# Performance work log

Hardware: AMD Instinct MI355X
Metric: run time of the kernel (lower is better)

## Reference

```python
import jax, jax.numpy as jnp
import numpy as np

EPS = 1e-6


def setup_inputs() -> dict:
    key = jax.random.key(0)
    k1, k2, k3, k4, k5, k6 = jax.random.split(key, 6)
    B, S = 32, 1024
    H, W = 32, 32            # max_n_patches_h/w
    C, P = 3, 16             # channels, patch_res
    D = C * P * P            # 768
    P2 = P * P               # 256
    patches = jax.random.normal(k1, (B, S, D), dtype=jnp.float32)
    pos_h = jax.random.randint(k2, (B, S), 0, H)
    pos_w = jax.random.randint(k3, (B, S), 0, W)
    key_pad_mask = jax.random.bernoulli(k4, 0.1, (B, S))  # True where padding
    n = jnp.zeros((H, W), dtype=jnp.float32)
    mean = 0.1 * jax.random.normal(k5, (H, W, P2), dtype=jnp.float32)
    m2 = jax.random.uniform(k6, (H, W, P2), dtype=jnp.float32)
    return {"patches": patches, "pos_h": pos_h, "pos_w": pos_w,
            "key_pad_mask": key_pad_mask, "n": n, "mean": mean, "m2": m2}


def reference(patches, pos_h, pos_w, key_pad_mask, n, mean, m2):
    """PatchNorm.forward in training mode (Welford update + normalize).

    Masked (padded) positions contribute 0 to the scatter sums and are
    written back as zeros, matching the torch boolean-mask gather/scatter.
    """
    H, W, P2 = mean.shape
    B, S, D = patches.shape
    C = D // P2
    HW = H * W

    x = patches.reshape(B * S, C, P2)                    # (N, c, p^2)
    pf = (pos_h * W + pos_w).reshape(-1)                 # (N,) flat grid index
    w = (~key_pad_mask).reshape(-1).astype(patches.dtype)  # 1.0 on valid tokens

    # --- Welford online update (torch scatter_add semantics w/ duplicates) ---
    counts = jax.ops.segment_sum(w, pf, num_segments=HW)
    n_new = n + counts.reshape(H, W)

    mean_flat = mean.reshape(HW, P2)
    delta = (x - mean_flat[pf][:, None, :]).mean(axis=1) * w[:, None]  # (N, p^2)
    n_g = jnp.maximum(n_new.reshape(HW)[pf], 1.0)
    mean_new_flat = mean_flat + jax.ops.segment_sum(delta / n_g[:, None], pf, num_segments=HW)
    mean_new = mean_new_flat.reshape(H, W, P2)

    delta2 = (x - mean_new_flat[pf][:, None, :]).mean(axis=1) * w[:, None]
    m2_new = m2 + jax.ops.segment_sum(delta * delta2, pf, num_segments=HW).reshape(H, W, P2)

    # --- var / std (var := 1 where n < 2) ---
    var = jnp.where((n_new < 2.0)[..., None], 1.0,
                    m2_new / jnp.maximum(n_new, 1.0)[..., None])
    std = jnp.sqrt(var)

    # --- normalize with gathered per-position stats, zero out padding ---
    mg = mean_new.reshape(HW, P2)[pf][:, None, :]        # (N, 1, p^2)
    sg = std.reshape(HW, P2)[pf][:, None, :]
    out = (x - mg) / (sg + EPS) * w[:, None, None]
    return out.reshape(B, S, D)
```

## Files before the change

### kernel.cpp

```cpp
#include <hip/hip_runtime.h>
#include <math.h>


#define EPSF 1e-6f

static constexpr int W_GRID  = 32;
static constexpr int P2      = 256;
static constexpr int P4      = 64;
static constexpr int D4      = 192;
static constexpr int HW      = 1024;
static constexpr int NTOK    = 32768;
static constexpr int LISTCAP = 96;
static constexpr int SLICE   = NTOK / HW;

__global__ void k_pf(const int* __restrict__ pos_h,
                     const int* __restrict__ pos_w,
                     const int* __restrict__ mask,
                     unsigned short* __restrict__ pf16) {
    int i = blockIdx.x * blockDim.x + threadIdx.x;
    if (i >= NTOK) return;
    const int valid = (mask[i] == 0);
    pf16[i] = valid ? (unsigned short)(pos_h[i] * W_GRID + pos_w[i])
                    : (unsigned short)0xFFFF;
}

__global__ void __launch_bounds__(256, 4)
k_cell(const float4* __restrict__ patches4,
       const unsigned short* __restrict__ pf16,
       const float* __restrict__ n_old,
       const float* __restrict__ mean_old,
       const float* __restrict__ m2_old,
       float4* __restrict__ out4) {
    const int g    = blockIdx.x;
    const int tid  = threadIdx.x;
    const int wave = tid >> 6;
    const int lane = tid & 63;

    __shared__ int            list[LISTCAP];
    __shared__ int            s_cnt;
    __shared__ unsigned short s_slice[SLICE];
    __shared__ float4         l14[4][64];
    __shared__ float4         l24[4][64];
    __shared__ float4         mn_s[P4];
    __shared__ float4         is_s[P4];

    if (tid == 0) s_cnt = 0;
    if (tid < SLICE) s_slice[tid] = pf16[g * SLICE + tid];

    const int4* pp = (const int4*)pf16;
    int4 v[16];
#pragma unroll
    for (int it = 0; it < 16; ++it) v[it] = pp[it * 256 + tid];

    __syncthreads();

#pragma unroll
    for (int t = 0; t < SLICE; ++t) {
        if (s_slice[t] == 0xFFFF) {
            const int i = g * SLICE + t;
            if (tid < D4)
                out4[(size_t)i * D4 + tid] = make_float4(0.f, 0.f, 0.f, 0.f);
        }
    }

#pragma unroll
    for (int it = 0; it < 16; ++it) {
        const int base = (it * 256 + tid) * 8;
#pragma unroll
        for (int k = 0; k < 4; ++k) {
            const int word = (&v[it].x)[k];
            const int g0 = word & 0xFFFF;
            const int g1 = (word >> 16) & 0xFFFF;
            if (g0 == g) { int s = atomicAdd(&s_cnt, 1); if (s < LISTCAP) list[s] = base + 2 * k; }
            if (g1 == g) { int s = atomicAdd(&s_cnt, 1); if (s < LISTCAP) list[s] = base + 2 * k + 1; }
        }
    }
    __syncthreads();
    const int c = min(s_cnt, LISTCAP);

    float4 s1 = make_float4(0.f, 0.f, 0.f, 0.f);
    float4 s2 = make_float4(0.f, 0.f, 0.f, 0.f);
    for (int k = wave; k < c; k += 32) {
        int   idx[8];
        float wf[8];
#pragma unroll
        for (int j = 0; j < 8; ++j) {
            const int  kk  = k + 4 * j;
            const bool val = (kk < c);
            wf[j]  = val ? 1.0f : 0.0f;
            idx[j] = list[val ? kk : k];
        }
        float4 A[8], Bv[8], Dv[8];
#pragma unroll
        for (int j = 0; j < 8; ++j) {
            const float4* tp = patches4 + (size_t)idx[j] * D4 + lane;
            A[j]  = tp[0];
            Bv[j] = tp[P4];
            Dv[j] = tp[2 * P4];
        }
        __builtin_amdgcn_sched_barrier(0);
#pragma unroll
        for (int j = 0; j < 8; ++j) {
            const float f = (1.0f / 3.0f) * wf[j];
            float4 xb;
            xb.x = (A[j].x + Bv[j].x + Dv[j].x) * f;
            xb.y = (A[j].y + Bv[j].y + Dv[j].y) * f;
            xb.z = (A[j].z + Bv[j].z + Dv[j].z) * f;
            xb.w = (A[j].w + Bv[j].w + Dv[j].w) * f;
            s1.x += xb.x; s1.y += xb.y; s1.z += xb.z; s1.w += xb.w;
            s2.x += xb.x * xb.x; s2.y += xb.y * xb.y;
            s2.z += xb.z * xb.z; s2.w += xb.w * xb.w;
        }
    }

    l14[wave][lane] = s1;
    l24[wave][lane] = s2;
    __syncthreads();

    {
        const float* l1f = (const float*)l14;
        const float* l2f = (const float*)l24;
        const float S1 = l1f[tid] + l1f[256 + tid] + l1f[512 + tid] + l1f[768 + tid];
        const float S2 = l2f[tid] + l2f[256 + tid] + l2f[512 + tid] + l2f[768 + tid];

        const float cnt = (float)c;
        const float nn  = n_old[g] + cnt;
        const float ng  = fmaxf(nn, 1.0f);
        const int   j   = g * P2 + tid;
        const float mo  = mean_old[j];
        const float mn  = mo + (S1 - cnt * mo) / ng;
        const float m2n = m2_old[j] + (S2 - (mo + mn) * S1 + cnt * mo * mn);
        const float var = (nn < 2.0f) ? 1.0f : (m2n / ng);
        ((float*)mn_s)[tid] = mn;
        ((float*)is_s)[tid] = 1.0f / (sqrtf(var) + EPSF);
    }
    __syncthreads();

    const float4 m4 = mn_s[lane];
    const float4 s4 = is_s[lane];
    for (int k = wave; k < c; k += 16) {
        int  idx[4];
        bool val[4];
#pragma unroll
        for (int j = 0; j < 4; ++j) {
            const int kk = k + 4 * j;
            val[j] = (kk < c);
            idx[j] = list[val[j] ? kk : k];
        }
        float4 X[12];
#pragma unroll
        for (int j = 0; j < 4; ++j) {
            const float4* tp = patches4 + (size_t)idx[j] * D4 + lane;
            X[3 * j]     = tp[0];
            X[3 * j + 1] = tp[P4];
            X[3 * j + 2] = tp[2 * P4];
        }
        __builtin_amdgcn_sched_barrier(0);
#pragma unroll
        for (int j = 0; j < 4; ++j) {
            if (val[j]) {
                float4* op = out4 + (size_t)idx[j] * D4 + lane;
                float4 r;
                r.x = (X[3 * j].x - m4.x) * s4.x;
                r.y = (X[3 * j].y - m4.y) * s4.y;
                r.z = (X[3 * j].z - m4.z) * s4.z;
                r.w = (X[3 * j].w - m4.w) * s4.w;
                op[0] = r;
                r.x = (X[3 * j + 1].x - m4.x) * s4.x;
                r.y = (X[3 * j + 1].y - m4.y) * s4.y;
                r.z = (X[3 * j + 1].z - m4.z) * s4.z;
                r.w = (X[3 * j + 1].w - m4.w) * s4.w;
                op[P4] = r;
                r.x = (X[3 * j + 2].x - m4.x) * s4.x;
                r.y = (X[3 * j + 2].y - m4.y) * s4.y;
                r.z = (X[3 * j + 2].z - m4.z) * s4.z;
                r.w = (X[3 * j + 2].w - m4.w) * s4.w;
                op[2 * P4] = r;
            }
        }
    }
}

extern "C" void kernel_launch(void* const* d_in, const int* in_sizes, int n_in,
                              void* d_out, int out_size, void* d_ws, size_t ws_size,
                              hipStream_t stream) {
    const float4* patches4 = (const float4*)d_in[0];
    const int*    pos_h    = (const int*)d_in[1];
    const int*    pos_w    = (const int*)d_in[2];
    const int*    mask     = (const int*)d_in[3];
    const float*  n_old    = (const float*)d_in[4];
    const float*  mean     = (const float*)d_in[5];
    const float*  m2       = (const float*)d_in[6];
    float4* out4 = (float4*)d_out;

    unsigned short* pf16 = (unsigned short*)d_ws;

    k_pf<<<NTOK / 256, 256, 0, stream>>>(pos_h, pos_w, mask, pf16);
    k_cell<<<HW, 256, 0, stream>>>(patches4, pf16, n_old, mean, m2, out4);
}
```

Measured before the change: 59.39 us.

## Stream statistics-pass patch rows into LDS with double-buffered direct loads

```diff
diff --git a/kernel.cpp b/kernel.cpp
--- a/kernel.cpp
+++ b/kernel.cpp
@@ -8,10 +8,14 @@
 static constexpr int P2      = 256;
 static constexpr int P4      = 64;
 static constexpr int D4      = 192;
+static constexpr int DDIM    = 768;
 static constexpr int HW      = 1024;
 static constexpr int NTOK    = 32768;
 static constexpr int LISTCAP = 96;
 static constexpr int SLICE   = NTOK / HW;
+
+typedef const __attribute__((address_space(1))) void gas_void;
+typedef __attribute__((address_space(3))) void       las_void;
 
 __global__ void k_pf(const int* __restrict__ pos_h,
                      const int* __restrict__ pos_w,
@@ -39,6 +43,7 @@
     __shared__ int            list[LISTCAP];
     __shared__ int            s_cnt;
     __shared__ unsigned short s_slice[SLICE];
+    __shared__ float          stage_lds[4][2][DDIM];
     __shared__ float4         l14[4][64];
     __shared__ float4         l24[4][64];
     __shared__ float4         mn_s[P4];
@@ -78,40 +83,46 @@
     __syncthreads();
     const int c = min(s_cnt, LISTCAP);
 
+    const int nr = (c > wave) ? ((c - wave + 3) >> 2) : 0;
+    float*   my_stage = &stage_lds[wave][0][0];
+
+    #define ISSUE_ROW(r)                                                      \
+    do {                                                                      \
+        const int kk_  = wave + 4 * (r);                                      \
+        const int idx_ = list[kk_];                                           \
+        const float* gb_ = ((const float*)patches4) + (size_t)idx_ * DDIM     \
+                           + lane * 4;                                        \
+        float* lb_ = my_stage + ((r) & 1) * DDIM;                             \
+        __builtin_amdgcn_global_load_lds((gas_void*)(gb_),       (las_void*)(lb_),       16, 0, 0); \
+        __builtin_amdgcn_global_load_lds((gas_void*)(gb_ + 256), (las_void*)(lb_ + 256), 16, 0, 0); \
+        __builtin_amdgcn_global_load_lds((gas_void*)(gb_ + 512), (las_void*)(lb_ + 512), 16, 0, 0); \
+    } while (0)
+
+    if (nr > 0) ISSUE_ROW(0);
+    if (nr > 1) ISSUE_ROW(1);
+
     float4 s1 = make_float4(0.f, 0.f, 0.f, 0.f);
     float4 s2 = make_float4(0.f, 0.f, 0.f, 0.f);
-    for (int k = wave; k < c; k += 32) {
-        int   idx[8];
-        float wf[8];
-#pragma unroll
-        for (int j = 0; j < 8; ++j) {
-            const int  kk  = k + 4 * j;
-            const bool val = (kk < c);
-            wf[j]  = val ? 1.0f : 0.0f;
-            idx[j] = list[val ? kk : k];
-        }
-        float4 A[8], Bv[8], Dv[8];
-#pragma unroll
-        for (int j = 0; j < 8; ++j) {
-            const float4* tp = patches4 + (size_t)idx[j] * D4 + lane;
-            A[j]  = tp[0];
-            Bv[j] = tp[P4];
-            Dv[j] = tp[2 * P4];
-        }
+    for (int r = 0; r < nr; ++r) {
+        if (r + 1 < nr) { asm volatile("s_waitcnt vmcnt(3)" ::: "memory"); }
+        else            { asm volatile("s_waitcnt vmcnt(0)" ::: "memory"); }
         __builtin_amdgcn_sched_barrier(0);
-#pragma unroll
-        for (int j = 0; j < 8; ++j) {
-            const float f = (1.0f / 3.0f) * wf[j];
-            float4 xb;
-            xb.x = (A[j].x + Bv[j].x + Dv[j].x) * f;
-            xb.y = (A[j].y + Bv[j].y + Dv[j].y) * f;
-            xb.z = (A[j].z + Bv[j].z + Dv[j].z) * f;
-            xb.w = (A[j].w + Bv[j].w + Dv[j].w) * f;
-            s1.x += xb.x; s1.y += xb.y; s1.z += xb.z; s1.w += xb.w;
-            s2.x += xb.x * xb.x; s2.y += xb.y * xb.y;
-            s2.z += xb.z * xb.z; s2.w += xb.w * xb.w;
-        }
-    }
+        const float4* row = (const float4*)(my_stage + (r & 1) * DDIM);
+        const float4 a = row[lane];
+        const float4 b = row[lane + 64];
+        const float4 d = row[lane + 128];
+        float4 xb;
+        xb.x = (a.x + b.x + d.x) * (1.0f / 3.0f);
+        xb.y = (a.y + b.y + d.y) * (1.0f / 3.0f);
+        xb.z = (a.z + b.z + d.z) * (1.0f / 3.0f);
+        xb.w = (a.w + b.w + d.w) * (1.0f / 3.0f);
+        s1.x += xb.x; s1.y += xb.y; s1.z += xb.z; s1.w += xb.w;
+        s2.x += xb.x * xb.x; s2.y += xb.y * xb.y;
+        s2.z += xb.z * xb.z; s2.w += xb.w * xb.w;
+        __builtin_amdgcn_sched_barrier(0);
+        if (r + 2 < nr) ISSUE_ROW(r + 2);
+    }
+    #undef ISSUE_ROW
 
     l14[wave][lane] = s1;
     l24[wave][lane] = s2;
```

Measured after the change: 58.57 us. About the same (-1.4%).

## Build per-cell token lists with a global atomic fill kernel instead of per-block scans

Applied to the files above, without the earlier changes.

```diff
diff --git a/kernel.cpp b/kernel.cpp
--- a/kernel.cpp
+++ b/kernel.cpp
@@ -4,29 +4,44 @@
 
 #define EPSF 1e-6f
 
-static constexpr int W_GRID  = 32;
-static constexpr int P2      = 256;
-static constexpr int P4      = 64;
-static constexpr int D4      = 192;
-static constexpr int HW      = 1024;
-static constexpr int NTOK    = 32768;
-static constexpr int LISTCAP = 96;
-static constexpr int SLICE   = NTOK / HW;
+static constexpr int W_GRID = 32;
+static constexpr int P2     = 256;
+static constexpr int P4     = 64;
+static constexpr int D4     = 192;
+static constexpr int HW     = 1024;
+static constexpr int NTOK   = 32768;
+static constexpr int MAXTOK = 128;
+static constexpr int SLICE  = NTOK / HW;
 
 __global__ void k_pf(const int* __restrict__ pos_h,
                      const int* __restrict__ pos_w,
                      const int* __restrict__ mask,
-                     unsigned short* __restrict__ pf16) {
-    int i = blockIdx.x * blockDim.x + threadIdx.x;
+                     unsigned short* __restrict__ pf16,
+                     int* __restrict__ cnt) {
+    const int i = blockIdx.x * blockDim.x + threadIdx.x;
+    if (i < HW) cnt[i] = 0;
     if (i >= NTOK) return;
     const int valid = (mask[i] == 0);
     pf16[i] = valid ? (unsigned short)(pos_h[i] * W_GRID + pos_w[i])
                     : (unsigned short)0xFFFF;
 }
 
-__global__ void __launch_bounds__(256, 4)
+__global__ void k_fill(const unsigned short* __restrict__ pf16,
+                       int* __restrict__ cnt,
+                       int* __restrict__ list) {
+    const int i = blockIdx.x * blockDim.x + threadIdx.x;
+    if (i >= NTOK) return;
+    const int g = pf16[i];
+    if (g == 0xFFFF) return;
+    const int slot = atomicAdd(&cnt[g], 1);
+    if (slot < MAXTOK) list[g * MAXTOK + slot] = i;
+}
+
+__global__ void __launch_bounds__(256, 8)
 k_cell(const float4* __restrict__ patches4,
        const unsigned short* __restrict__ pf16,
+       const int* __restrict__ cnt,
+       const int* __restrict__ list_g,
        const float* __restrict__ n_old,
        const float* __restrict__ mean_old,
        const float* __restrict__ m2_old,
@@ -36,22 +51,16 @@
     const int wave = tid >> 6;
     const int lane = tid & 63;
 
-    __shared__ int            list[LISTCAP];
-    __shared__ int            s_cnt;
+    __shared__ int            list[MAXTOK];
     __shared__ unsigned short s_slice[SLICE];
     __shared__ float4         l14[4][64];
     __shared__ float4         l24[4][64];
     __shared__ float4         mn_s[P4];
     __shared__ float4         is_s[P4];
 
-    if (tid == 0) s_cnt = 0;
+    const int c = min(cnt[g], MAXTOK);
+    if (tid < c) list[tid] = list_g[g * MAXTOK + tid];
     if (tid < SLICE) s_slice[tid] = pf16[g * SLICE + tid];
-
-    const int4* pp = (const int4*)pf16;
-    int4 v[16];
-#pragma unroll
-    for (int it = 0; it < 16; ++it) v[it] = pp[it * 256 + tid];
-
     __syncthreads();
 
 #pragma unroll
@@ -63,50 +72,34 @@
         }
     }
 
-#pragma unroll
-    for (int it = 0; it < 16; ++it) {
-        const int base = (it * 256 + tid) * 8;
-#pragma unroll
-        for (int k = 0; k < 4; ++k) {
-            const int word = (&v[it].x)[k];
-            const int g0 = word & 0xFFFF;
-            const int g1 = (word >> 16) & 0xFFFF;
-            if (g0 == g) { int s = atomicAdd(&s_cnt, 1); if (s < LISTCAP) list[s] = base + 2 * k; }
-            if (g1 == g) { int s = atomicAdd(&s_cnt, 1); if (s < LISTCAP) list[s] = base + 2 * k + 1; }
-        }
-    }
-    __syncthreads();
-    const int c = min(s_cnt, LISTCAP);
-
     float4 s1 = make_float4(0.f, 0.f, 0.f, 0.f);
     float4 s2 = make_float4(0.f, 0.f, 0.f, 0.f);
-    for (int k = wave; k < c; k += 32) {
-        int   idx[8];
-        float wf[8];
+    for (int k = wave; k < c; k += 16) {
+        int   idx[4];
+        float wf[4];
 #pragma unroll
-        for (int j = 0; j < 8; ++j) {
+        for (int j = 0; j < 4; ++j) {
             const int  kk  = k + 4 * j;
             const bool val = (kk < c);
             wf[j]  = val ? 1.0f : 0.0f;
             idx[j] = list[val ? kk : k];
         }
-        float4 A[8], Bv[8], Dv[8];
+        float4 A[4], B[4], Dd[4];
 #pragma unroll
-        for (int j = 0; j < 8; ++j) {
+        for (int j = 0; j < 4; ++j) {
             const float4* tp = patches4 + (size_t)idx[j] * D4 + lane;
             A[j]  = tp[0];
-            Bv[j] = tp[P4];
-            Dv[j] = tp[2 * P4];
+            B[j]  = tp[P4];
+            Dd[j] = tp[2 * P4];
         }
-        __builtin_amdgcn_sched_barrier(0);
 #pragma unroll
-        for (int j = 0; j < 8; ++j) {
+        for (int j = 0; j < 4; ++j) {
             const float f = (1.0f / 3.0f) * wf[j];
             float4 xb;
-            xb.x = (A[j].x + Bv[j].x + Dv[j].x) * f;
-            xb.y = (A[j].y + Bv[j].y + Dv[j].y) * f;
-            xb.z = (A[j].z + Bv[j].z + Dv[j].z) * f;
-            xb.w = (A[j].w + Bv[j].w + Dv[j].w) * f;
+            xb.x = (A[j].x + B[j].x + Dd[j].x) * f;
+            xb.y = (A[j].y + B[j].y + Dd[j].y) * f;
+            xb.z = (A[j].z + B[j].z + Dd[j].z) * f;
+            xb.w = (A[j].w + B[j].w + Dd[j].w) * f;
             s1.x += xb.x; s1.y += xb.y; s1.z += xb.z; s1.w += xb.w;
             s2.x += xb.x * xb.x; s2.y += xb.y * xb.y;
             s2.z += xb.z * xb.z; s2.w += xb.w * xb.w;
@@ -123,14 +116,14 @@
         const float S1 = l1f[tid] + l1f[256 + tid] + l1f[512 + tid] + l1f[768 + tid];
         const float S2 = l2f[tid] + l2f[256 + tid] + l2f[512 + tid] + l2f[768 + tid];
 
-        const float cnt = (float)c;
-        const float nn  = n_old[g] + cnt;
-        const float ng  = fmaxf(nn, 1.0f);
-        const int   j   = g * P2 + tid;
-        const float mo  = mean_old[j];
-        const float mn  = mo + (S1 - cnt * mo) / ng;
-        const float m2n = m2_old[j] + (S2 - (mo + mn) * S1 + cnt * mo * mn);
-        const float var = (nn < 2.0f) ? 1.0f : (m2n / ng);
+        const float cntf = (float)c;
+        const float nn   = n_old[g] + cntf;
+        const float ng   = fmaxf(nn, 1.0f);
+        const int   j    = g * P2 + tid;
+        const float mo   = mean_old[j];
+        const float mn   = mo + (S1 - cntf * mo) / ng;
+        const float m2n  = m2_old[j] + (S2 - (mo + mn) * S1 + cntf * mo * mn);
+        const float var  = (nn < 2.0f) ? 1.0f : (m2n / ng);
         ((float*)mn_s)[tid] = mn;
         ((float*)is_s)[tid] = 1.0f / (sqrtf(var) + EPSF);
     }
@@ -155,7 +148,6 @@
             X[3 * j + 1] = tp[P4];
             X[3 * j + 2] = tp[2 * P4];
         }
-        __builtin_amdgcn_sched_barrier(0);
 #pragma unroll
         for (int j = 0; j < 4; ++j) {
             if (val[j]) {
@@ -194,7 +186,11 @@
     float4* out4 = (float4*)d_out;
 
     unsigned short* pf16 = (unsigned short*)d_ws;
+    int* cnt  = (int*)(pf16 + NTOK);
+    int* list = cnt + HW;
 
-    k_pf<<<NTOK / 256, 256, 0, stream>>>(pos_h, pos_w, mask, pf16);
-    k_cell<<<HW, 256, 0, stream>>>(patches4, pf16, n_old, mean, m2, out4);
+    k_pf<<<NTOK / 256, 256, 0, stream>>>(pos_h, pos_w, mask, pf16, cnt);
+    k_fill<<<NTOK / 256, 256, 0, stream>>>(pf16, cnt, list);
+    k_cell<<<HW, 256, 0, stream>>>(patches4, pf16, cnt, list,
+                                   n_old, mean, m2, out4);
 }
```

Result: slower. 62.45 us (+5.2%).

## Use nontemporal loads/stores for patch output and shrink stats batching

Applied to the files above, without the earlier changes.

```diff
diff --git a/kernel.cpp b/kernel.cpp
--- a/kernel.cpp
+++ b/kernel.cpp
@@ -3,6 +3,8 @@
 
 
 #define EPSF 1e-6f
+
+typedef float v4 __attribute__((ext_vector_type(4)));
 
 static constexpr int W_GRID  = 32;
 static constexpr int P2      = 256;
@@ -25,12 +27,12 @@
 }
 
 __global__ void __launch_bounds__(256, 4)
-k_cell(const float4* __restrict__ patches4,
+k_cell(const v4* __restrict__ patches4,
        const unsigned short* __restrict__ pf16,
        const float* __restrict__ n_old,
        const float* __restrict__ mean_old,
        const float* __restrict__ m2_old,
-       float4* __restrict__ out4) {
+       v4* __restrict__ out4) {
     const int g    = blockIdx.x;
     const int tid  = threadIdx.x;
     const int wave = tid >> 6;
@@ -39,10 +41,10 @@
     __shared__ int            list[LISTCAP];
     __shared__ int            s_cnt;
     __shared__ unsigned short s_slice[SLICE];
-    __shared__ float4         l14[4][64];
-    __shared__ float4         l24[4][64];
-    __shared__ float4         mn_s[P4];
-    __shared__ float4         is_s[P4];
+    __shared__ v4             l14[4][64];
+    __shared__ v4             l24[4][64];
+    __shared__ v4             mn_s[P4];
+    __shared__ v4             is_s[P4];
 
     if (tid == 0) s_cnt = 0;
     if (tid < SLICE) s_slice[tid] = pf16[g * SLICE + tid];
@@ -54,12 +56,13 @@
 
     __syncthreads();
 
+    const v4 zero4 = {0.f, 0.f, 0.f, 0.f};
 #pragma unroll
     for (int t = 0; t < SLICE; ++t) {
         if (s_slice[t] == 0xFFFF) {
             const int i = g * SLICE + t;
             if (tid < D4)
-                out4[(size_t)i * D4 + tid] = make_float4(0.f, 0.f, 0.f, 0.f);
+                __builtin_nontemporal_store(zero4, out4 + (size_t)i * D4 + tid);
         }
     }
 
@@ -78,38 +81,31 @@
     __syncthreads();
     const int c = min(s_cnt, LISTCAP);
 
-    float4 s1 = make_float4(0.f, 0.f, 0.f, 0.f);
-    float4 s2 = make_float4(0.f, 0.f, 0.f, 0.f);
-    for (int k = wave; k < c; k += 32) {
-        int   idx[8];
-        float wf[8];
+    v4 s1 = zero4;
+    v4 s2 = zero4;
+    for (int k = wave; k < c; k += 16) {
+        int   idx[4];
+        float wf[4];
 #pragma unroll
-        for (int j = 0; j < 8; ++j) {
+        for (int j = 0; j < 4; ++j) {
             const int  kk  = k + 4 * j;
             const bool val = (kk < c);
             wf[j]  = val ? 1.0f : 0.0f;
             idx[j] = list[val ? kk : k];
         }
-        float4 A[8], Bv[8], Dv[8];
+        v4 A[4], B[4], Dd[4];
 #pragma unroll
-        for (int j = 0; j < 8; ++j) {
-            const float4* tp = patches4 + (size_t)idx[j] * D4 + lane;
+        for (int j = 0; j < 4; ++j) {
+            const v4* tp = patches4 + (size_t)idx[j] * D4 + lane;
             A[j]  = tp[0];
-            Bv[j] = tp[P4];
-            Dv[j] = tp[2 * P4];
+            B[j]  = tp[P4];
+            Dd[j] = tp[2 * P4];
         }
-        __builtin_amdgcn_sched_barrier(0);
 #pragma unroll
-        for (int j = 0; j < 8; ++j) {
-            const float f = (1.0f / 3.0f) * wf[j];
-            float4 xb;
-            xb.x = (A[j].x + Bv[j].x + Dv[j].x) * f;
-            xb.y = (A[j].y + Bv[j].y + Dv[j].y) * f;
-            xb.z = (A[j].z + Bv[j].z + Dv[j].z) * f;
-            xb.w = (A[j].w + Bv[j].w + Dv[j].w) * f;
-            s1.x += xb.x; s1.y += xb.y; s1.z += xb.z; s1.w += xb.w;
-            s2.x += xb.x * xb.x; s2.y += xb.y * xb.y;
-            s2.z += xb.z * xb.z; s2.w += xb.w * xb.w;
+        for (int j = 0; j < 4; ++j) {
+            const v4 xb = (A[j] + B[j] + Dd[j]) * ((1.0f / 3.0f) * wf[j]);
+            s1 += xb;
+            s2 += xb * xb;
         }
     }
 
@@ -136,8 +132,8 @@
     }
     __syncthreads();
 
-    const float4 m4 = mn_s[lane];
-    const float4 s4 = is_s[lane];
+    const v4 m4 = mn_s[lane];
+    const v4 s4 = is_s[lane];
     for (int k = wave; k < c; k += 16) {
         int  idx[4];
         bool val[4];
@@ -147,35 +143,21 @@
             val[j] = (kk < c);
             idx[j] = list[val[j] ? kk : k];
         }
-        float4 X[12];
+        v4 X[12];
 #pragma unroll
         for (int j = 0; j < 4; ++j) {
-            const float4* tp = patches4 + (size_t)idx[j] * D4 + lane;
-            X[3 * j]     = tp[0];
-            X[3 * j + 1] = tp[P4];
-            X[3 * j + 2] = tp[2 * P4];
+            const v4* tp = patches4 + (size_t)idx[j] * D4 + lane;
+            X[3 * j]     = __builtin_nontemporal_load(tp);
+            X[3 * j + 1] = __builtin_nontemporal_load(tp + P4);
+            X[3 * j + 2] = __builtin_nontemporal_load(tp + 2 * P4);
         }
-        __builtin_amdgcn_sched_barrier(0);
 #pragma unroll
         for (int j = 0; j < 4; ++j) {
             if (val[j]) {
-                float4* op = out4 + (size_t)idx[j] * D4 + lane;
-                float4 r;
-                r.x = (X[3 * j].x - m4.x) * s4.x;
-                r.y = (X[3 * j].y - m4.y) * s4.y;
-                r.z = (X[3 * j].z - m4.z) * s4.z;
-                r.w = (X[3 * j].w - m4.w) * s4.w;
-                op[0] = r;
-                r.x = (X[3 * j + 1].x - m4.x) * s4.x;
-                r.y = (X[3 * j + 1].y - m4.y) * s4.y;
-                r.z = (X[3 * j + 1].z - m4.z) * s4.z;
-                r.w = (X[3 * j + 1].w - m4.w) * s4.w;
-                op[P4] = r;
-                r.x = (X[3 * j + 2].x - m4.x) * s4.x;
-                r.y = (X[3 * j + 2].y - m4.y) * s4.y;
-                r.z = (X[3 * j + 2].z - m4.z) * s4.z;
-                r.w = (X[3 * j + 2].w - m4.w) * s4.w;
-                op[2 * P4] = r;
+                v4* op = out4 + (size_t)idx[j] * D4 + lane;
+                __builtin_nontemporal_store((X[3 * j]     - m4) * s4, op);
+                __builtin_nontemporal_store((X[3 * j + 1] - m4) * s4, op + P4);
+                __builtin_nontemporal_store((X[3 * j + 2] - m4) * s4, op + 2 * P4);
             }
         }
     }
@@ -184,14 +166,14 @@
 extern "C" void kernel_launch(void* const* d_in, const int* in_sizes, int n_in,
                               void* d_out, int out_size, void* d_ws, size_t ws_size,
                               hipStream_t stream) {
-    const float4* patches4 = (const float4*)d_in[0];
-    const int*    pos_h    = (const int*)d_in[1];
-    const int*    pos_w    = (const int*)d_in[2];
-    const int*    mask     = (const int*)d_in[3];
-    const float*  n_old    = (const float*)d_in[4];
-    const float*  mean     = (const float*)d_in[5];
-    const float*  m2       = (const float*)d_in[6];
-    float4* out4 = (float4*)d_out;
+    const v4*  patches4 = (const v4*)d_in[0];
+    const int* pos_h    = (const int*)d_in[1];
+    const int* pos_w    = (const int*)d_in[2];
+    const int* mask     = (const int*)d_in[3];
+    const float* n_old  = (const float*)d_in[4];
+    const float* mean   = (const float*)d_in[5];
+    const float* m2     = (const float*)d_in[6];
+    v4* out4 = (v4*)d_out;
 
     unsigned short* pf16 = (unsigned short*)d_ws;
 
```

Measured after the change: 57.08 us. 3.9% less time.
